# Kernel optimization log

Measured on AMD Instinct MI355X. Metric: run time of the kernel, lower is better.

The kernel has to match this reference:

```python
import jax, jax.numpy as jnp
import numpy as np

EMBED = 256      # embedding_dim
HEADS = 4        # attn_heads
OUT = EMBED // HEADS  # out_channels per head = 64
R = 8            # n_relations = len(metapaths) + 1
N = 16384        # num_nodes
NEG_SLOPE = 0.2  # PyG GATv2 default leaky_relu slope


def setup_inputs() -> dict:
    key = jax.random.key(0)
    ks = jax.random.split(key, 16)
    s = 0.05
    inp = {"relation_embs": jax.random.normal(ks[0], (N, R, EMBED), jnp.float32)}
    # Two GATv2Conv layers: lin_l (src), lin_r (dst), att vector, output bias.
    for i in range(2):
        inp[f"Wl{i}"] = jax.random.normal(ks[1 + 6 * i], (EMBED, HEADS, OUT), jnp.float32) * s
        inp[f"bl{i}"] = jax.random.normal(ks[2 + 6 * i], (HEADS, OUT), jnp.float32) * s
        inp[f"Wr{i}"] = jax.random.normal(ks[3 + 6 * i], (EMBED, HEADS, OUT), jnp.float32) * s
        inp[f"br{i}"] = jax.random.normal(ks[4 + 6 * i], (HEADS, OUT), jnp.float32) * s
        inp[f"att{i}"] = jax.random.normal(ks[5 + 6 * i], (HEADS, OUT), jnp.float32) * s
        inp[f"bias{i}"] = jax.random.normal(ks[6 + 6 * i], (HEADS * OUT,), jnp.float32) * s
    return inp


def reference(relation_embs, Wl0, bl0, Wr0, br0, att0, bias0,
              Wl1, bl1, Wr1, br1, att1, bias1):
    # Each node owns a fully-connected graph over its R relation embeddings
    # (all rows nonzero under randn fill), so the PyG gather/softmax/scatter
    # collapses to dense [N, R_dst, R_src] attention.
    h = jax.nn.relu(relation_embs)                                  # [N,R,D]

    # ---- GATv2 layer 0: full FC edges (every src -> every dst) ----
    xl = jnp.einsum('nrd,dhc->nrhc', h, Wl0) + bl0                  # src feats [N,R,H,C]
    xr = jnp.einsum('nrd,dhc->nrhc', h, Wr0) + br0                  # dst feats [N,R,H,C]
    e = jax.nn.leaky_relu(xr[:, :, None] + xl[:, None], NEG_SLOPE)  # [N,Ri,Rj,H,C]
    logits = jnp.einsum('nijhc,hc->nijh', e, att0)                  # [N,Ri,Rj,H]
    alpha = jax.nn.softmax(logits, axis=2)                          # softmax over src j
    h = jnp.einsum('nijh,njhc->nihc', alpha, xl)                    # [N,R,H,C]
    h = h.reshape(N, R, HEADS * OUT) + bias0
    h = jax.nn.relu(h)

    # ---- GATv2 layer 1 (last): only edges into the self node (nid == R-1) ----
    xl = jnp.einsum('nrd,dhc->nrhc', h, Wl1) + bl1                  # src feats [N,R,H,C]
    xr_self = jnp.einsum('nd,dhc->nhc', h[:, -1], Wr1) + br1        # dst = self [N,H,C]
    e = jax.nn.leaky_relu(xr_self[:, None] + xl, NEG_SLOPE)         # [N,R,H,C]
    logits = jnp.einsum('nrhc,hc->nrh', e, att1)                    # [N,R,H]
    alpha = jax.nn.softmax(logits, axis=1)                          # softmax over src r
    out = jnp.einsum('nrh,nrhc->nhc', alpha, xl).reshape(N, HEADS * OUT) + bias1
    node_embs = jax.nn.relu(out)                                    # [N, D]

    # betas: last-layer attention into the self node, detached (SparseTensor.to_dense().detach())
    betas = jax.lax.stop_gradient(alpha)                            # [N,R,H]
    return node_embs, betas
```

## Files before the change

kernel.cpp:

```cpp
#include <hip/hip_runtime.h>


#define NNODES 16384
#define NB 4
#define MR 32

typedef _Float16 f16x8 __attribute__((ext_vector_type(8)));
typedef _Float16 f16x4 __attribute__((ext_vector_type(4)));
typedef _Float16 f16x2 __attribute__((ext_vector_type(2)));
typedef float f32x4 __attribute__((ext_vector_type(4)));

#if __has_builtin(__builtin_amdgcn_fdot2)
#define FDOT2(a, b, c) __builtin_amdgcn_fdot2((a), (b), (c), false)
#else
#define FDOT2(a, b, c) ((c) + (float)(a)[0] * (float)(b)[0] + (float)(a)[1] * (float)(b)[1])
#endif

__device__ __forceinline__ f16x2 leaky2(f16x2 t) {
#if __has_builtin(__builtin_elementwise_max)
    return __builtin_elementwise_max(t, t * (f16x2){(_Float16)0.2f, (_Float16)0.2f});
#else
    const unsigned u = __builtin_bit_cast(unsigned, t) & 0x7FFF7FFFu;
    const f16x2 at = __builtin_bit_cast(f16x2, u);
    return t * (f16x2){(_Float16)0.6f, (_Float16)0.6f} +
           at * (f16x2){(_Float16)0.4f, (_Float16)0.4f};
#endif
}
__device__ __forceinline__ f16x2 relu2(f16x2 t) {
#if __has_builtin(__builtin_elementwise_max)
    return __builtin_elementwise_max(t, (f16x2){(_Float16)0.f, (_Float16)0.f});
#else
    const unsigned u = __builtin_bit_cast(unsigned, t) & 0x7FFF7FFFu;
    const f16x2 at = __builtin_bit_cast(f16x2, u);
    return (t + at) * (f16x2){(_Float16)0.5f, (_Float16)0.5f};
#endif
}

__device__ __forceinline__ int swz(int row, int chunk) {
    return row * 256 + ((chunk ^ (row & 7)) << 3);
}

__global__ void prep_weights(const float* __restrict__ Wl0, const float* __restrict__ Wr0,
                             const float* __restrict__ Wl1, const float* __restrict__ Wr1,
                             _Float16* __restrict__ wt) {
    __shared__ float tile[64 * 68];
    const int t  = threadIdx.x;
    const int m  = blockIdx.x >> 4;
    const int kt = (blockIdx.x >> 2) & 3;
    const int nt = blockIdx.x & 3;
    const float* src = (m == 0 ? Wl0 : m == 1 ? Wr0 : m == 2 ? Wl1 : Wr1) + kt * 64 * 256;
    #pragma unroll
    for (int i = 0; i < 4; ++i) {
        const int idx = i * 256 + t;
        const int kk  = idx >> 4;
        const int nn  = (idx & 15) * 4;
        const float4 v = *(const float4*)&src[kk * 256 + nt * 64 + nn];
        tile[kk * 68 + nn + 0] = v.x;
        tile[kk * 68 + nn + 1] = v.y;
        tile[kk * 68 + nn + 2] = v.z;
        tile[kk * 68 + nn + 3] = v.w;
    }
    __syncthreads();
    const int n  = t >> 2;
    const int ks = (t & 3) * 16;
    f16x8 o0, o1;
    #pragma unroll
    for (int e = 0; e < 8; ++e) o0[e] = (_Float16)tile[(ks + e) * 68 + n];
    #pragma unroll
    for (int e = 0; e < 8; ++e) o1[e] = (_Float16)tile[(ks + 8 + e) * 68 + n];
    _Float16* dst = &wt[(size_t)(m * 256 + nt * 64 + n) * 256 + kt * 64 + ks];
    *(f16x8*)dst = o0;
    *(f16x8*)(dst + 8) = o1;
}

__launch_bounds__(256, 4)
__global__ void gat_fused(const float* __restrict__ x,
                          const float* __restrict__ bl0, const float* __restrict__ br0,
                          const float* __restrict__ att0, const float* __restrict__ bias0,
                          const float* __restrict__ bl1, const float* __restrict__ br1,
                          const float* __restrict__ att1, const float* __restrict__ bias1,
                          const _Float16* __restrict__ wt,
                          float* __restrict__ out) {
    __shared__ _Float16 bufA[MR * 256];
    __shared__ _Float16 bufB[MR * 256];
    __shared__ _Float16 aw[MR * 4 * 8];
    __shared__ _Float16 xrsH[NB * 256];
    __shared__ float lgs[NB * 32];
    __shared__ float al1[NB * 32];
    __shared__ _Float16 attH[768];

    const int tid  = threadIdx.x;
    const int bg   = blockIdx.x;
    const int lane = tid & 63;
    const int wv   = tid >> 6;
    const int lr   = lane & 15;
    const int lq   = lane >> 4;

    {
        const float4* src = (const float4*)(x + (size_t)bg * (MR * 256));
        #pragma unroll
        for (int it = 0; it < 4; ++it) {
            const int g   = it * 256 + tid;
            const int row = g >> 5;
            const int c   = g & 31;
            const float4 v0 = src[2 * g];
            const float4 v1 = src[2 * g + 1];
            f16x8 s;
            s[0] = (_Float16)fmaxf(v0.x, 0.f); s[1] = (_Float16)fmaxf(v0.y, 0.f);
            s[2] = (_Float16)fmaxf(v0.z, 0.f); s[3] = (_Float16)fmaxf(v0.w, 0.f);
            s[4] = (_Float16)fmaxf(v1.x, 0.f); s[5] = (_Float16)fmaxf(v1.y, 0.f);
            s[6] = (_Float16)fmaxf(v1.z, 0.f); s[7] = (_Float16)fmaxf(v1.w, 0.f);
            *(f16x8*)&bufA[swz(row, c)] = s;
        }
        attH[tid]       = (_Float16)att0[tid];
        attH[256 + tid] = (_Float16)att1[tid];
        attH[512 + tid] = (_Float16)bias0[tid];
    }
    __syncthreads();

    {
        f32x4 acc[2][8];
        #pragma unroll
        for (int m = 0; m < 2; ++m)
            #pragma unroll
            for (int n = 0; n < 8; ++n)
                acc[m][n] = f32x4{0.f, 0.f, 0.f, 0.f};
        #pragma unroll
        for (int kt = 0; kt < 8; ++kt) {
            f16x8 a[2], b[8];
            #pragma unroll
            for (int m = 0; m < 2; ++m)
                a[m] = *(const f16x8*)&bufA[swz(m * 16 + lr, kt * 4 + lq)];
            const int koff = kt * 32 + lq * 8;
            #pragma unroll
            for (int n = 0; n < 8; ++n)
                b[n] = *(const f16x8*)&wt[(size_t)(wv * 128 + n * 16 + lr) * 256 + koff];
            #pragma unroll
            for (int m = 0; m < 2; ++m)
                #pragma unroll
                for (int n = 0; n < 8; ++n)
                    acc[m][n] = __builtin_amdgcn_mfma_f32_16x16x32_f16(a[m], b[n], acc[m][n], 0, 0, 0);
        }
        __syncthreads();
        _Float16* dstbuf = (wv < 2) ? bufB : bufA;
        const float* bv = (wv < 2) ? bl0 : br0;
        #pragma unroll
        for (int n = 0; n < 8; ++n) {
            const int cl   = (wv & 1) * 128 + n * 16 + lr;
            const float bias = bv[cl];
            const int ch   = cl >> 3, ce = cl & 7;
            #pragma unroll
            for (int m = 0; m < 2; ++m)
                #pragma unroll
                for (int r = 0; r < 4; ++r) {
                    const int row = m * 16 + lq * 4 + r;
                    dstbuf[swz(row, ch) + ce] = (_Float16)(acc[m][n][r] + bias);
                }
        }
    }
    __syncthreads();

    {
        const int n  = tid >> 6;
        const int i  = (tid >> 3) & 7;
        const int h  = (tid >> 1) & 3;
        const int jh = tid & 1;
        const int rowR = n * 8 + i;
        f16x2 xr2[32];
        #pragma unroll
        for (int cc = 0; cc < 8; ++cc) {
            const int c3 = (cc + 2 * h) & 7;
            const f16x8 v = *(const f16x8*)&bufA[swz(rowR, h * 8 + c3)];
            xr2[cc * 4 + 0] = f16x2{v[0], v[1]};
            xr2[cc * 4 + 1] = f16x2{v[2], v[3]};
            xr2[cc * 4 + 2] = f16x2{v[4], v[5]};
            xr2[cc * 4 + 3] = f16x2{v[6], v[7]};
        }
        f16x8 lbuf[2][4];
        f16x8 abuf[2];
        {
            const int c3 = (2 * h) & 7;
            abuf[0] = *(const f16x8*)&attH[h * 64 + c3 * 8];
            #pragma unroll
            for (int jj = 0; jj < 4; ++jj)
                lbuf[0][jj] = *(const f16x8*)&bufB[swz(n * 8 + jh * 4 + jj, h * 8 + c3)];
        }
        float lg[4] = {0.f, 0.f, 0.f, 0.f};
        #pragma unroll
        for (int cc = 0; cc < 8; ++cc) {
            const int cur = cc & 1, nxt = cur ^ 1;
            if (cc < 7) {
                const int c3n = (cc + 1 + 2 * h) & 7;
                abuf[nxt] = *(const f16x8*)&attH[h * 64 + c3n * 8];
                #pragma unroll
                for (int jj = 0; jj < 4; ++jj)
                    lbuf[nxt][jj] = *(const f16x8*)&bufB[swz(n * 8 + jh * 4 + jj, h * 8 + c3n)];
            }
            const f16x8 a8 = abuf[cur];
            const f16x2 a2[4] = {{a8[0], a8[1]}, {a8[2], a8[3]}, {a8[4], a8[5]}, {a8[6], a8[7]}};
            #pragma unroll
            for (int jj = 0; jj < 4; ++jj) {
                const f16x8 l8 = lbuf[cur][jj];
                const f16x2 l2[4] = {{l8[0], l8[1]}, {l8[2], l8[3]}, {l8[4], l8[5]}, {l8[6], l8[7]}};
                #pragma unroll
                for (int p = 0; p < 4; ++p) {
                    const f16x2 t = leaky2(xr2[cc * 4 + p] + l2[p]);
                    lg[jj] = FDOT2(t, a2[p], lg[jj]);
                }
            }
        }
        float mx = fmaxf(fmaxf(lg[0], lg[1]), fmaxf(lg[2], lg[3]));
        mx = fmaxf(mx, __shfl_xor(mx, 1));
        float ex[4], ssum = 0.f;
        #pragma unroll
        for (int jj = 0; jj < 4; ++jj) { ex[jj] = __expf(lg[jj] - mx); ssum += ex[jj]; }
        const float tot = ssum + __shfl_xor(ssum, 1);
        const float inv = 1.f / tot;
        f16x4 w;
        #pragma unroll
        for (int jj = 0; jj < 4; ++jj) w[jj] = (_Float16)(ex[jj] * inv);
        *(f16x4*)&aw[((n * 8 + i) * 4 + h) * 8 + jh * 4] = w;
    }
    __syncthreads();

    {
        const int row  = tid >> 3;
        const int sub  = tid & 7;
        const int h    = sub >> 1;
        const int half = sub & 1;
        const int nn   = row >> 3;
        const int cb   = h * 8 + half * 4;
        const f16x8 ah8 = *(const f16x8*)&aw[(row * 4 + h) * 8];
        f16x2 acc2[16];
        #pragma unroll
        for (int p = 0; p < 16; ++p) acc2[p] = (f16x2){(_Float16)0.f, (_Float16)0.f};
        f16x8 vbuf[2][4];
        #pragma unroll
        for (int cc = 0; cc < 4; ++cc)
            vbuf[0][cc] = *(const f16x8*)&bufB[swz(nn * 8, cb + ((cc + h) & 3))];
        #pragma unroll
        for (int j = 0; j < 8; ++j) {
            const int cur = j & 1, nxt = cur ^ 1;
            if (j < 7) {
                #pragma unroll
                for (int cc = 0; cc < 4; ++cc)
                    vbuf[nxt][cc] = *(const f16x8*)&bufB[swz(nn * 8 + j + 1, cb + ((cc + h) & 3))];
            }
            const f16x2 a2 = {ah8[j], ah8[j]};
            #pragma unroll
            for (int cc = 0; cc < 4; ++cc) {
                const f16x8 v = vbuf[cur][cc];
                acc2[cc * 4 + 0] += f16x2{v[0], v[1]} * a2;
                acc2[cc * 4 + 1] += f16x2{v[2], v[3]} * a2;
                acc2[cc * 4 + 2] += f16x2{v[4], v[5]} * a2;
                acc2[cc * 4 + 3] += f16x2{v[6], v[7]} * a2;
            }
        }
        #pragma unroll
        for (int cc = 0; cc < 4; ++cc) {
            const int c = cb + ((cc + h) & 3);
            const f16x8 b8 = *(const f16x8*)&attH[512 + c * 8];
            f16x8 s;
            #pragma unroll
            for (int p = 0; p < 4; ++p) {
                const f16x2 r = relu2(acc2[cc * 4 + p] + f16x2{b8[2 * p], b8[2 * p + 1]});
                s[2 * p]     = r[0];
                s[2 * p + 1] = r[1];
            }
            *(f16x8*)&bufA[swz(row, c)] = s;
        }
    }
    __syncthreads();

    {
        f32x4 accl[2][4], accr[4];
        #pragma unroll
        for (int m = 0; m < 2; ++m)
            #pragma unroll
            for (int n = 0; n < 4; ++n)
                accl[m][n] = f32x4{0.f, 0.f, 0.f, 0.f};
        #pragma unroll
        for (int n = 0; n < 4; ++n) accr[n] = f32x4{0.f, 0.f, 0.f, 0.f};
        const _Float16* W1l = wt + 512 * 256;
        const _Float16* W1r = wt + 768 * 256;
        const int rowS = (lr & 3) * 8 + 7;
        #pragma unroll
        for (int kt = 0; kt < 8; ++kt) {
            const int koff = kt * 32 + lq * 8;
            f16x8 a[2], as, bl[4], br[4];
            #pragma unroll
            for (int m = 0; m < 2; ++m)
                a[m] = *(const f16x8*)&bufA[swz(m * 16 + lr, kt * 4 + lq)];
            as = *(const f16x8*)&bufA[swz(rowS, kt * 4 + lq)];
            #pragma unroll
            for (int n = 0; n < 4; ++n) {
                bl[n] = *(const f16x8*)&W1l[(size_t)(wv * 64 + n * 16 + lr) * 256 + koff];
                br[n] = *(const f16x8*)&W1r[(size_t)(wv * 64 + n * 16 + lr) * 256 + koff];
            }
            #pragma unroll
            for (int m = 0; m < 2; ++m)
                #pragma unroll
                for (int n = 0; n < 4; ++n)
                    accl[m][n] = __builtin_amdgcn_mfma_f32_16x16x32_f16(a[m], bl[n], accl[m][n], 0, 0, 0);
            #pragma unroll
            for (int n = 0; n < 4; ++n)
                accr[n] = __builtin_amdgcn_mfma_f32_16x16x32_f16(as, br[n], accr[n], 0, 0, 0);
        }
        #pragma unroll
        for (int n = 0; n < 4; ++n) {
            const int col = wv * 64 + n * 16 + lr;
            const float b1 = bl1[col], b2 = br1[col];
            const int ch = col >> 3, ce = col & 7;
            #pragma unroll
            for (int m = 0; m < 2; ++m)
                #pragma unroll
                for (int r = 0; r < 4; ++r) {
                    const int row = m * 16 + lq * 4 + r;
                    bufB[swz(row, ch) + ce] = (_Float16)(accl[m][n][r] + b1);
                }
            if (lq == 0) {
                #pragma unroll
                for (int r = 0; r < 4; ++r)
                    xrsH[r * 256 + col] = (_Float16)(accr[n][r] + b2);
            }
        }
    }
    __syncthreads();

    {
        const int n  = tid >> 5;
        const int rr = (tid >> 2) & 7;
        const int h  = tid & 3;
        float lg = 0.f;
        if (tid < 128) {
            const int rowj = n * 8 + rr;
            f16x8 xbuf[2], lbuf[2], abuf[2];
            {
                const int c = h * 8 + ((2 * h) & 7);
                xbuf[0] = *(const f16x8*)&xrsH[n * 256 + c * 8];
                lbuf[0] = *(const f16x8*)&bufB[swz(rowj, c)];
                abuf[0] = *(const f16x8*)&attH[256 + c * 8];
            }
            #pragma unroll
            for (int cc = 0; cc < 8; ++cc) {
                const int cur = cc & 1, nxt = cur ^ 1;
                if (cc < 7) {
                    const int cn = h * 8 + ((cc + 1 + 2 * h) & 7);
                    xbuf[nxt] = *(const f16x8*)&xrsH[n * 256 + cn * 8];
                    lbuf[nxt] = *(const f16x8*)&bufB[swz(rowj, cn)];
                    abuf[nxt] = *(const f16x8*)&attH[256 + cn * 8];
                }
                const f16x8 x8 = xbuf[cur];
                const f16x8 l8 = lbuf[cur];
                const f16x8 a8 = abuf[cur];
                #pragma unroll
                for (int p = 0; p < 4; ++p) {
                    const f16x2 xp = {x8[2 * p], x8[2 * p + 1]};
                    const f16x2 lp = {l8[2 * p], l8[2 * p + 1]};
                    const f16x2 ap = {a8[2 * p], a8[2 * p + 1]};
                    const f16x2 t = leaky2(xp + lp);
                    lg = FDOT2(t, ap, lg);
                }
            }
            lgs[tid] = lg;
        }
        __syncthreads();
        if (tid < 128) {
            float M = -1e30f;
            float l[8];
            #pragma unroll
            for (int j = 0; j < 8; ++j) {
                l[j] = lgs[n * 32 + j * 4 + h];
                M = fmaxf(M, l[j]);
            }
            float S = 0.f;
            #pragma unroll
            for (int j = 0; j < 8; ++j) S += __expf(l[j] - M);
            const float a = __expf(lg - M) / S;
            al1[tid] = a;
            out[(size_t)NNODES * 256 + (size_t)(bg * NB + n) * 32 + rr * 4 + h] = a;
        }
    }
    __syncthreads();

    {
        const int n  = tid >> 6;
        const int q  = tid & 63;
        const int c0 = q * 4;
        const int h  = q >> 4;
        f16x4 v[8];
        float a[8];
        #pragma unroll
        for (int r = 0; r < 8; ++r) {
            v[r] = *(const f16x4*)&bufB[swz(n * 8 + r, q >> 1) + (q & 1) * 4];
            a[r] = al1[n * 32 + r * 4 + h];
        }
        float o0 = 0.f, o1 = 0.f, o2 = 0.f, o3 = 0.f;
        #pragma unroll
        for (int r = 0; r < 8; ++r) {
            o0 = fmaf((float)v[r][0], a[r], o0);
            o1 = fmaf((float)v[r][1], a[r], o1);
            o2 = fmaf((float)v[r][2], a[r], o2);
            o3 = fmaf((float)v[r][3], a[r], o3);
        }
        float4 res;
        res.x = fmaxf(o0 + bias1[c0 + 0], 0.f);
        res.y = fmaxf(o1 + bias1[c0 + 1], 0.f);
        res.z = fmaxf(o2 + bias1[c0 + 2], 0.f);
        res.w = fmaxf(o3 + bias1[c0 + 3], 0.f);
        *(float4*)&out[(size_t)(bg * NB + n) * 256 + c0] = res;
    }
}

extern "C" void kernel_launch(void* const* d_in, const int* in_sizes, int n_in,
                              void* d_out, int out_size, void* d_ws, size_t ws_size,
                              hipStream_t stream) {
    const float* x     = (const float*)d_in[0];
    const float* Wl0   = (const float*)d_in[1];
    const float* bl0   = (const float*)d_in[2];
    const float* Wr0   = (const float*)d_in[3];
    const float* br0   = (const float*)d_in[4];
    const float* att0  = (const float*)d_in[5];
    const float* bias0 = (const float*)d_in[6];
    const float* Wl1   = (const float*)d_in[7];
    const float* bl1   = (const float*)d_in[8];
    const float* Wr1   = (const float*)d_in[9];
    const float* br1   = (const float*)d_in[10];
    const float* att1  = (const float*)d_in[11];
    const float* bias1 = (const float*)d_in[12];
    _Float16* wt = (_Float16*)d_ws;
    float* out = (float*)d_out;

    prep_weights<<<64, 256, 0, stream>>>(Wl0, Wr0, Wl1, Wr1, wt);
    gat_fused<<<NNODES / NB, 256, 0, stream>>>(x, bl0, br0, att0, bias0,
                                               bl1, br1, att1, bias1, wt, out);
}
```

Before: 432.2 us.

## Double threads per block to 512 and split every stage's work across them

Launches the fused GAT kernel with 512 threads instead of 256 and repartitions every stage (input load, both MFMA projections, layer-0 logits, aggregation, final output) so each thread handles half the previous work. Per-thread register arrays shrink, which is meant to raise occupancy and latency hiding (launch bounds now 512,6). The tradeoff is more waves contending for the same LDS and barriers, smaller per-wave MFMA tiles that reload weight fragments more often, and narrower global stores.

```diff
diff --git a/kernel.cpp b/kernel.cpp
--- a/kernel.cpp
+++ b/kernel.cpp
@@ -73,7 +73,7 @@
     *(f16x8*)(dst + 8) = o1;
 }
 
-__launch_bounds__(256, 4)
+__launch_bounds__(512, 6)
 __global__ void gat_fused(const float* __restrict__ x,
                           const float* __restrict__ bl0, const float* __restrict__ br0,
                           const float* __restrict__ att0, const float* __restrict__ bias0,
@@ -99,8 +99,8 @@
     {
         const float4* src = (const float4*)(x + (size_t)bg * (MR * 256));
         #pragma unroll
-        for (int it = 0; it < 4; ++it) {
-            const int g   = it * 256 + tid;
+        for (int it = 0; it < 2; ++it) {
+            const int g   = it * 512 + tid;
             const int row = g >> 5;
             const int c   = g & 31;
             const float4 v0 = src[2 * g];
@@ -112,41 +112,44 @@
             s[6] = (_Float16)fmaxf(v1.z, 0.f); s[7] = (_Float16)fmaxf(v1.w, 0.f);
             *(f16x8*)&bufA[swz(row, c)] = s;
         }
-        attH[tid]       = (_Float16)att0[tid];
-        attH[256 + tid] = (_Float16)att1[tid];
-        attH[512 + tid] = (_Float16)bias0[tid];
-    }
-    __syncthreads();
-
-    {
-        f32x4 acc[2][8];
+        if (tid < 256) {
+            attH[tid]       = (_Float16)att0[tid];
+            attH[512 + tid] = (_Float16)bias0[tid];
+        } else {
+            attH[tid]       = (_Float16)att1[tid - 256];
+        }
+    }
+    __syncthreads();
+
+    {
+        f32x4 acc[2][4];
         #pragma unroll
         for (int m = 0; m < 2; ++m)
             #pragma unroll
-            for (int n = 0; n < 8; ++n)
+            for (int n = 0; n < 4; ++n)
                 acc[m][n] = f32x4{0.f, 0.f, 0.f, 0.f};
         #pragma unroll
         for (int kt = 0; kt < 8; ++kt) {
-            f16x8 a[2], b[8];
+            f16x8 a[2], b[4];
             #pragma unroll
             for (int m = 0; m < 2; ++m)
                 a[m] = *(const f16x8*)&bufA[swz(m * 16 + lr, kt * 4 + lq)];
             const int koff = kt * 32 + lq * 8;
             #pragma unroll
-            for (int n = 0; n < 8; ++n)
-                b[n] = *(const f16x8*)&wt[(size_t)(wv * 128 + n * 16 + lr) * 256 + koff];
-            #pragma unroll
-            for (int m = 0; m < 2; ++m)
-                #pragma unroll
-                for (int n = 0; n < 8; ++n)
+            for (int n = 0; n < 4; ++n)
+                b[n] = *(const f16x8*)&wt[(size_t)(wv * 64 + n * 16 + lr) * 256 + koff];
+            #pragma unroll
+            for (int m = 0; m < 2; ++m)
+                #pragma unroll
+                for (int n = 0; n < 4; ++n)
                     acc[m][n] = __builtin_amdgcn_mfma_f32_16x16x32_f16(a[m], b[n], acc[m][n], 0, 0, 0);
         }
         __syncthreads();
-        _Float16* dstbuf = (wv < 2) ? bufB : bufA;
-        const float* bv = (wv < 2) ? bl0 : br0;
-        #pragma unroll
-        for (int n = 0; n < 8; ++n) {
-            const int cl   = (wv & 1) * 128 + n * 16 + lr;
+        _Float16* dstbuf = (wv < 4) ? bufB : bufA;
+        const float* bv = (wv < 4) ? bl0 : br0;
+        #pragma unroll
+        for (int n = 0; n < 4; ++n) {
+            const int cl   = (wv & 3) * 64 + n * 16 + lr;
             const float bias = bv[cl];
             const int ch   = cl >> 3, ce = cl & 7;
             #pragma unroll
@@ -161,109 +164,98 @@
     __syncthreads();
 
     {
-        const int n  = tid >> 6;
-        const int i  = (tid >> 3) & 7;
-        const int h  = (tid >> 1) & 3;
-        const int jh = tid & 1;
+        const int n  = tid >> 7;
+        const int i  = (tid >> 4) & 7;
+        const int h  = (tid >> 2) & 3;
+        const int jh = tid & 3;
         const int rowR = n * 8 + i;
-        f16x2 xr2[32];
-        #pragma unroll
-        for (int cc = 0; cc < 8; ++cc) {
-            const int c3 = (cc + 2 * h) & 7;
-            const f16x8 v = *(const f16x8*)&bufA[swz(rowR, h * 8 + c3)];
-            xr2[cc * 4 + 0] = f16x2{v[0], v[1]};
-            xr2[cc * 4 + 1] = f16x2{v[2], v[3]};
-            xr2[cc * 4 + 2] = f16x2{v[4], v[5]};
-            xr2[cc * 4 + 3] = f16x2{v[6], v[7]};
-        }
-        f16x8 lbuf[2][4];
-        f16x8 abuf[2];
+        const int j0 = jh * 2, j1 = jh * 2 + 1;
+        f16x8 xrb[2], ab[2], lb0[2], lb1[2];
         {
-            const int c3 = (2 * h) & 7;
-            abuf[0] = *(const f16x8*)&attH[h * 64 + c3 * 8];
-            #pragma unroll
-            for (int jj = 0; jj < 4; ++jj)
-                lbuf[0][jj] = *(const f16x8*)&bufB[swz(n * 8 + jh * 4 + jj, h * 8 + c3)];
-        }
-        float lg[4] = {0.f, 0.f, 0.f, 0.f};
+            const int c3 = (2 * h + i) & 7;
+            xrb[0] = *(const f16x8*)&bufA[swz(rowR, h * 8 + c3)];
+            ab[0]  = *(const f16x8*)&attH[h * 64 + c3 * 8];
+            lb0[0] = *(const f16x8*)&bufB[swz(n * 8 + j0, h * 8 + c3)];
+            lb1[0] = *(const f16x8*)&bufB[swz(n * 8 + j1, h * 8 + c3)];
+        }
+        float lgA = 0.f, lgB = 0.f;
         #pragma unroll
         for (int cc = 0; cc < 8; ++cc) {
             const int cur = cc & 1, nxt = cur ^ 1;
             if (cc < 7) {
-                const int c3n = (cc + 1 + 2 * h) & 7;
-                abuf[nxt] = *(const f16x8*)&attH[h * 64 + c3n * 8];
-                #pragma unroll
-                for (int jj = 0; jj < 4; ++jj)
-                    lbuf[nxt][jj] = *(const f16x8*)&bufB[swz(n * 8 + jh * 4 + jj, h * 8 + c3n)];
-            }
-            const f16x8 a8 = abuf[cur];
-            const f16x2 a2[4] = {{a8[0], a8[1]}, {a8[2], a8[3]}, {a8[4], a8[5]}, {a8[6], a8[7]}};
-            #pragma unroll
-            for (int jj = 0; jj < 4; ++jj) {
-                const f16x8 l8 = lbuf[cur][jj];
-                const f16x2 l2[4] = {{l8[0], l8[1]}, {l8[2], l8[3]}, {l8[4], l8[5]}, {l8[6], l8[7]}};
-                #pragma unroll
-                for (int p = 0; p < 4; ++p) {
-                    const f16x2 t = leaky2(xr2[cc * 4 + p] + l2[p]);
-                    lg[jj] = FDOT2(t, a2[p], lg[jj]);
-                }
-            }
-        }
-        float mx = fmaxf(fmaxf(lg[0], lg[1]), fmaxf(lg[2], lg[3]));
+                const int c3n = (cc + 1 + 2 * h + i) & 7;
+                xrb[nxt] = *(const f16x8*)&bufA[swz(rowR, h * 8 + c3n)];
+                ab[nxt]  = *(const f16x8*)&attH[h * 64 + c3n * 8];
+                lb0[nxt] = *(const f16x8*)&bufB[swz(n * 8 + j0, h * 8 + c3n)];
+                lb1[nxt] = *(const f16x8*)&bufB[swz(n * 8 + j1, h * 8 + c3n)];
+            }
+            const f16x8 x8 = xrb[cur];
+            const f16x8 a8 = ab[cur];
+            const f16x8 u8 = lb0[cur];
+            const f16x8 w8 = lb1[cur];
+            #pragma unroll
+            for (int p = 0; p < 4; ++p) {
+                const f16x2 xp = {x8[2 * p], x8[2 * p + 1]};
+                const f16x2 apv = {a8[2 * p], a8[2 * p + 1]};
+                const f16x2 t0 = leaky2(xp + f16x2{u8[2 * p], u8[2 * p + 1]});
+                const f16x2 t1 = leaky2(xp + f16x2{w8[2 * p], w8[2 * p + 1]});
+                lgA = FDOT2(t0, apv, lgA);
+                lgB = FDOT2(t1, apv, lgB);
+            }
+        }
+        float mx = fmaxf(lgA, lgB);
         mx = fmaxf(mx, __shfl_xor(mx, 1));
-        float ex[4], ssum = 0.f;
-        #pragma unroll
-        for (int jj = 0; jj < 4; ++jj) { ex[jj] = __expf(lg[jj] - mx); ssum += ex[jj]; }
-        const float tot = ssum + __shfl_xor(ssum, 1);
-        const float inv = 1.f / tot;
-        f16x4 w;
-        #pragma unroll
-        for (int jj = 0; jj < 4; ++jj) w[jj] = (_Float16)(ex[jj] * inv);
-        *(f16x4*)&aw[((n * 8 + i) * 4 + h) * 8 + jh * 4] = w;
-    }
-    __syncthreads();
-
-    {
-        const int row  = tid >> 3;
-        const int sub  = tid & 7;
-        const int h    = sub >> 1;
-        const int half = sub & 1;
-        const int nn   = row >> 3;
-        const int cb   = h * 8 + half * 4;
+        mx = fmaxf(mx, __shfl_xor(mx, 2));
+        const float exA = __expf(lgA - mx), exB = __expf(lgB - mx);
+        float ssum = exA + exB;
+        ssum += __shfl_xor(ssum, 1);
+        ssum += __shfl_xor(ssum, 2);
+        const float inv = 1.f / ssum;
+        const f16x2 w = {(_Float16)(exA * inv), (_Float16)(exB * inv)};
+        *(f16x2*)&aw[(rowR * 4 + h) * 8 + jh * 2] = w;
+    }
+    __syncthreads();
+
+    {
+        const int row = tid >> 4;
+        const int sub = tid & 15;
+        const int h   = sub >> 2;
+        const int q   = sub & 3;
+        const int nn  = row >> 3;
+        const int cA  = h * 8 + ((q + 2 * h) & 7);
+        const int cB  = h * 8 + ((q + 2 * h + 4) & 7);
         const f16x8 ah8 = *(const f16x8*)&aw[(row * 4 + h) * 8];
-        f16x2 acc2[16];
-        #pragma unroll
-        for (int p = 0; p < 16; ++p) acc2[p] = (f16x2){(_Float16)0.f, (_Float16)0.f};
-        f16x8 vbuf[2][4];
-        #pragma unroll
-        for (int cc = 0; cc < 4; ++cc)
-            vbuf[0][cc] = *(const f16x8*)&bufB[swz(nn * 8, cb + ((cc + h) & 3))];
+        f16x2 acc2[8];
+        #pragma unroll
+        for (int p = 0; p < 8; ++p) acc2[p] = (f16x2){(_Float16)0.f, (_Float16)0.f};
+        f16x8 vb[2][2];
+        vb[0][0] = *(const f16x8*)&bufB[swz(nn * 8, cA)];
+        vb[0][1] = *(const f16x8*)&bufB[swz(nn * 8, cB)];
         #pragma unroll
         for (int j = 0; j < 8; ++j) {
             const int cur = j & 1, nxt = cur ^ 1;
             if (j < 7) {
-                #pragma unroll
-                for (int cc = 0; cc < 4; ++cc)
-                    vbuf[nxt][cc] = *(const f16x8*)&bufB[swz(nn * 8 + j + 1, cb + ((cc + h) & 3))];
+                vb[nxt][0] = *(const f16x8*)&bufB[swz(nn * 8 + j + 1, cA)];
+                vb[nxt][1] = *(const f16x8*)&bufB[swz(nn * 8 + j + 1, cB)];
             }
             const f16x2 a2 = {ah8[j], ah8[j]};
             #pragma unroll
-            for (int cc = 0; cc < 4; ++cc) {
-                const f16x8 v = vbuf[cur][cc];
-                acc2[cc * 4 + 0] += f16x2{v[0], v[1]} * a2;
-                acc2[cc * 4 + 1] += f16x2{v[2], v[3]} * a2;
-                acc2[cc * 4 + 2] += f16x2{v[4], v[5]} * a2;
-                acc2[cc * 4 + 3] += f16x2{v[6], v[7]} * a2;
-            }
-        }
-        #pragma unroll
-        for (int cc = 0; cc < 4; ++cc) {
-            const int c = cb + ((cc + h) & 3);
+            for (int k = 0; k < 2; ++k) {
+                const f16x8 v = vb[cur][k];
+                acc2[k * 4 + 0] += f16x2{v[0], v[1]} * a2;
+                acc2[k * 4 + 1] += f16x2{v[2], v[3]} * a2;
+                acc2[k * 4 + 2] += f16x2{v[4], v[5]} * a2;
+                acc2[k * 4 + 3] += f16x2{v[6], v[7]} * a2;
+            }
+        }
+        #pragma unroll
+        for (int k = 0; k < 2; ++k) {
+            const int c = k ? cB : cA;
             const f16x8 b8 = *(const f16x8*)&attH[512 + c * 8];
             f16x8 s;
             #pragma unroll
             for (int p = 0; p < 4; ++p) {
-                const f16x2 r = relu2(acc2[cc * 4 + p] + f16x2{b8[2 * p], b8[2 * p + 1]});
+                const f16x2 r = relu2(acc2[k * 4 + p] + f16x2{b8[2 * p], b8[2 * p + 1]});
                 s[2 * p]     = r[0];
                 s[2 * p + 1] = r[1];
             }
@@ -273,42 +265,42 @@
     __syncthreads();
 
     {
-        f32x4 accl[2][4], accr[4];
+        f32x4 accl[2][2], accr[2];
         #pragma unroll
         for (int m = 0; m < 2; ++m)
             #pragma unroll
-            for (int n = 0; n < 4; ++n)
+            for (int n = 0; n < 2; ++n)
                 accl[m][n] = f32x4{0.f, 0.f, 0.f, 0.f};
         #pragma unroll
-        for (int n = 0; n < 4; ++n) accr[n] = f32x4{0.f, 0.f, 0.f, 0.f};
+        for (int n = 0; n < 2; ++n) accr[n] = f32x4{0.f, 0.f, 0.f, 0.f};
         const _Float16* W1l = wt + 512 * 256;
         const _Float16* W1r = wt + 768 * 256;
         const int rowS = (lr & 3) * 8 + 7;
         #pragma unroll
         for (int kt = 0; kt < 8; ++kt) {
             const int koff = kt * 32 + lq * 8;
-            f16x8 a[2], as, bl[4], br[4];
+            f16x8 a[2], as, bl[2], br[2];
             #pragma unroll
             for (int m = 0; m < 2; ++m)
                 a[m] = *(const f16x8*)&bufA[swz(m * 16 + lr, kt * 4 + lq)];
             as = *(const f16x8*)&bufA[swz(rowS, kt * 4 + lq)];
             #pragma unroll
-            for (int n = 0; n < 4; ++n) {
-                bl[n] = *(const f16x8*)&W1l[(size_t)(wv * 64 + n * 16 + lr) * 256 + koff];
-                br[n] = *(const f16x8*)&W1r[(size_t)(wv * 64 + n * 16 + lr) * 256 + koff];
-            }
-            #pragma unroll
-            for (int m = 0; m < 2; ++m)
-                #pragma unroll
-                for (int n = 0; n < 4; ++n)
+            for (int n = 0; n < 2; ++n) {
+                bl[n] = *(const f16x8*)&W1l[(size_t)(wv * 32 + n * 16 + lr) * 256 + koff];
+                br[n] = *(const f16x8*)&W1r[(size_t)(wv * 32 + n * 16 + lr) * 256 + koff];
+            }
+            #pragma unroll
+            for (int m = 0; m < 2; ++m)
+                #pragma unroll
+                for (int n = 0; n < 2; ++n)
                     accl[m][n] = __builtin_amdgcn_mfma_f32_16x16x32_f16(a[m], bl[n], accl[m][n], 0, 0, 0);
             #pragma unroll
-            for (int n = 0; n < 4; ++n)
+            for (int n = 0; n < 2; ++n)
                 accr[n] = __builtin_amdgcn_mfma_f32_16x16x32_f16(as, br[n], accr[n], 0, 0, 0);
         }
         #pragma unroll
-        for (int n = 0; n < 4; ++n) {
-            const int col = wv * 64 + n * 16 + lr;
+        for (int n = 0; n < 2; ++n) {
+            const int col = wv * 32 + n * 16 + lr;
             const float b1 = bl1[col], b2 = br1[col];
             const int ch = col >> 3, ce = col & 7;
             #pragma unroll
@@ -384,31 +376,27 @@
     __syncthreads();
 
     {
-        const int n  = tid >> 6;
-        const int q  = tid & 63;
-        const int c0 = q * 4;
-        const int h  = q >> 4;
-        f16x4 v[8];
+        const int n  = tid >> 7;
+        const int q  = tid & 127;
+        const int c0 = q * 2;
+        const int h  = q >> 5;
+        f16x2 v[8];
         float a[8];
         #pragma unroll
         for (int r = 0; r < 8; ++r) {
-            v[r] = *(const f16x4*)&bufB[swz(n * 8 + r, q >> 1) + (q & 1) * 4];
+            v[r] = *(const f16x2*)&bufB[swz(n * 8 + r, q >> 2) + (q & 3) * 2];
             a[r] = al1[n * 32 + r * 4 + h];
         }
-        float o0 = 0.f, o1 = 0.f, o2 = 0.f, o3 = 0.f;
+        float o0 = 0.f, o1 = 0.f;
         #pragma unroll
         for (int r = 0; r < 8; ++r) {
             o0 = fmaf((float)v[r][0], a[r], o0);
             o1 = fmaf((float)v[r][1], a[r], o1);
-            o2 = fmaf((float)v[r][2], a[r], o2);
-            o3 = fmaf((float)v[r][3], a[r], o3);
-        }
-        float4 res;
+        }
+        float2 res;
         res.x = fmaxf(o0 + bias1[c0 + 0], 0.f);
         res.y = fmaxf(o1 + bias1[c0 + 1], 0.f);
-        res.z = fmaxf(o2 + bias1[c0 + 2], 0.f);
-        res.w = fmaxf(o3 + bias1[c0 + 3], 0.f);
-        *(float4*)&out[(size_t)(bg * NB + n) * 256 + c0] = res;
+        *(float2*)&out[(size_t)(bg * NB + n) * 256 + c0] = res;
     }
 }
 
@@ -432,6 +420,6 @@
     float* out = (float*)d_out;
 
     prep_weights<<<64, 256, 0, stream>>>(Wl0, Wr0, Wl1, Wr1, wt);
-    gat_fused<<<NNODES / NB, 256, 0, stream>>>(x, bl0, br0, att0, bias0,
+    gat_fused<<<NNODES / NB, 512, 0, stream>>>(x, bl0, br0, att0, bias0,
                                                bl1, br1, att1, bias1, wt, out);
 }
```

Result: slower. 454.3 us (+5.1%).
